# Optimization experiments

Hardware: AMD Instinct MI355X
Metric: run time of the kernel (lower is better)

## Reference

```python
import jax, jax.numpy as jnp
import numpy as np

B, S, D = 8, 1024, 1024
H, HD = 16, 64  # multiheads, head_dim; H*HD == D


def setup_inputs() -> dict:
    key = jax.random.key(0)
    ks = jax.random.split(key, 6)
    mk = lambda k, shape, scale=1.0: (jax.random.normal(k, shape, dtype=jnp.float32) * scale)
    return {
        "Q_seq": mk(ks[0], (B, S, D)),
        "K_seq": mk(ks[1], (B, S, D)),
        "V_seq": mk(ks[2], (B, S, D)),
        # nn.Linear weights stored as (out_features, in_features)
        "WQ": mk(ks[3], (H * HD, D), scale=D ** -0.5),
        "WK": mk(ks[4], (H * HD, D), scale=D ** -0.5),
        "WV": mk(ks[5], (H * HD, D), scale=D ** -0.5),
    }


def _attn(Q_seq, K_seq, V_seq, WQ, WK, WV):
    # projections (Linear: x @ W.T), then split heads -> [B, H, S, HD]
    def proj(x, W):
        y = jnp.einsum('bsd,od->bso', x, W)
        return y.reshape(x.shape[0], -1, H, HD).transpose(0, 2, 1, 3)
    Q, K, V = proj(Q_seq, WQ), proj(K_seq, WK), proj(V_seq, WV)
    scale = 1.0 / jnp.sqrt(jnp.float32(HD))
    scores = jnp.einsum('bhqd,bhkd->bhqk', Q, K) * scale  # [B,H,S,S]
    attn = jax.nn.softmax(scores, axis=-1)
    # dropout p=0.1 is identity in eval mode
    out = jnp.einsum('bhqk,bhkd->bhqd', attn, V)
    return out.transpose(0, 2, 1, 3).reshape(out.shape[0], -1, H * HD)


def reference(Q_seq, K_seq, V_seq, WQ, WK, WV):
    return _attn(Q_seq, K_seq, V_seq, WQ, WK, WV)
```

## Files before the change

kernel.cpp:

```cpp
#include <hip/hip_runtime.h>
#include <stdint.h>


#define B_N 8
#define S_N 1024
#define D_N 1024
#define H_N 16
#define HD_N 64
#define M_N (B_N * S_N)

typedef __bf16 bfrag __attribute__((ext_vector_type(8)));
typedef float f32x4 __attribute__((ext_vector_type(4)));
typedef float f32x16 __attribute__((ext_vector_type(16)));
typedef unsigned int u32;
typedef u32 u32x2 __attribute__((ext_vector_type(2)));
typedef unsigned short u16;

__device__ __forceinline__ u16 f2bf(float f) {
  uint32_t u = __float_as_uint(f);
  u += 0x7FFFu + ((u >> 16) & 1u);
  return (u16)(u >> 16);
}

__device__ __forceinline__ void gl_lds16(const void* g, void* l) {
  __builtin_amdgcn_global_load_lds(
      (const __attribute__((address_space(1))) uint32_t*)g,
      (__attribute__((address_space(3))) uint32_t*)l, 16, 0, 0);
}

__device__ __forceinline__ u32 cvtpk(float lo, float hi) {
  u32 r;
  asm("v_cvt_pk_bf16_f32 %0, %1, %2" : "=v"(r) : "v"(lo), "v"(hi));
  return r;
}

__device__ __forceinline__ u32x2 pl32swap(u32 a, u32 b) {
#if __has_builtin(__builtin_amdgcn_permlane32_swap)
  return __builtin_amdgcn_permlane32_swap(a, b, false, false);
#else
  u32 sa = (u32)__shfl_xor((int)a, 32, 64), sb = (u32)__shfl_xor((int)b, 32, 64);
  const bool hi = (threadIdx.x & 32) != 0;
  u32x2 r;
  r[0] = hi ? sb : a;
  r[1] = hi ? b : sa;
  return r;
#endif
}

__device__ __forceinline__ float xhalf_max(float v) {
  u32x2 r = pl32swap(__float_as_uint(v), __float_as_uint(v));
  return fmaxf(__uint_as_float(r[0]), __uint_as_float(r[1]));
}
__device__ __forceinline__ float xhalf_add(float v) {
  u32x2 r = pl32swap(__float_as_uint(v), __float_as_uint(v));
  return __uint_as_float(r[0]) + __uint_as_float(r[1]);
}

__global__ void cvt3(const float* __restrict__ s0, const float* __restrict__ s1,
                     const float* __restrict__ s2, u16* __restrict__ d0,
                     u16* __restrict__ d1, u16* __restrict__ d2, int n4) {
  const float* s = blockIdx.y == 0 ? s0 : (blockIdx.y == 1 ? s1 : s2);
  u16* d = blockIdx.y == 0 ? d0 : (blockIdx.y == 1 ? d1 : d2);
  int i = blockIdx.x * 256 + threadIdx.x;
  if (i < n4) {
    float4 v = ((const float4*)s)[i];
    ushort4 o;
    o.x = f2bf(v.x); o.y = f2bf(v.y); o.z = f2bf(v.z); o.w = f2bf(v.w);
    ((ushort4*)d)[i] = o;
  }
}

__global__ __launch_bounds__(512, 1) void gemm_qkv(const u16* __restrict__ Xbf,
                                                   const u16* __restrict__ Wbf,
                                                   u16* __restrict__ Ybf) {
  const int bid = blockIdx.x;
  const int wid = (bid & 7) * 96 + (bid >> 3);
  const int mat = wid >> 8;
  const int rem = wid & 255;
  const int m0 = (rem >> 3) * 256;
  const int n0 = (rem & 7) * 128;

  const u16* A = Xbf + (size_t)mat * (M_N * D_N);
  const u16* Bw = Wbf + (size_t)mat * (D_N * D_N);
  u16* Y = Ybf + (size_t)mat * (M_N * D_N);

  __shared__ u16 Ast[3][4][4096];
  __shared__ u16 Bst[3][2][4096];

  const int t = threadIdx.x;
  const int w = t >> 6, l = t & 63;
  const int lr = l & 15, lg = l >> 4;
  const int wm = w >> 1, wn = w & 1;

  const int swcol = (((t & 7) ^ ((t >> 3) & 7)) << 3);
  const u16* aSrc = A + (size_t)(m0 + (t >> 3)) * D_N + swcol;
  const u16* bSrc = Bw + (size_t)(n0 + (t >> 3)) * D_N + swcol;

  const int asw = (lr & 7) << 3;
  const int koff0 = (lg * 8) ^ asw;
  const int koff1 = (32 + lg * 8) ^ asw;

#define STA(buf, c, tt)                                                       \
  gl_lds16(aSrc + (size_t)((c)*64) * D_N + (tt)*64, &Ast[buf][c][t * 8])
#define STB(buf, c, tt)                                                       \
  gl_lds16(bSrc + (size_t)((c)*64) * D_N + (tt)*64, &Bst[buf][c][t * 8])
#define LDA8(AR, buf)                                                         \
  do {                                                                        \
    const u16* p_ = &Ast[buf][wm][lr * 64];                                   \
    _Pragma("unroll") for (int mf_ = 0; mf_ < 4; ++mf_) {                     \
      AR[mf_][0] = *(const bfrag*)(p_ + mf_ * 1024 + koff0);                  \
      AR[mf_][1] = *(const bfrag*)(p_ + mf_ * 1024 + koff1);                  \
    }                                                                         \
  } while (0)
#define LDB4(BR, buf, h)                                                      \
  do {                                                                        \
    const u16* p_ = &Bst[buf][wn][((h)*32 + lr) * 64];                        \
    BR[0][0] = *(const bfrag*)(p_ + koff0);                                   \
    BR[0][1] = *(const bfrag*)(p_ + koff1);                                   \
    BR[1][0] = *(const bfrag*)(p_ + 1024 + koff0);                            \
    BR[1][1] = *(const bfrag*)(p_ + 1024 + koff1);                            \
  } while (0)
#define MMAH(h, AR, BR)                                                       \
  do {                                                                        \
    __builtin_amdgcn_s_setprio(1);                                            \
    _Pragma("unroll") for (int mf_ = 0; mf_ < 4; ++mf_)                       \
    _Pragma("unroll") for (int j_ = 0; j_ < 2; ++j_)                          \
    _Pragma("unroll") for (int kk_ = 0; kk_ < 2; ++kk_)                       \
      acc[mf_][(h)*2 + j_] = __builtin_amdgcn_mfma_f32_16x16x32_bf16(         \
          AR[mf_][kk_], BR[j_][kk_], acc[mf_][(h)*2 + j_], 0, 0, 0);          \
    __builtin_amdgcn_s_setprio(0);                                            \
  } while (0)
#define BARR()                                                                \
  __builtin_amdgcn_s_barrier();                                               \
  __builtin_amdgcn_sched_barrier(0)
#define WAITL()                                                               \
  asm volatile("s_waitcnt lgkmcnt(0)" ::: "memory");                          \
  __builtin_amdgcn_sched_barrier(0)
#define WAITV(n)                                                              \
  asm volatile("s_waitcnt vmcnt(" #n ")" ::: "memory");                       \
  __builtin_amdgcn_sched_barrier(0)

  f32x4 acc[4][4];
#pragma unroll
  for (int i = 0; i < 4; ++i)
#pragma unroll
    for (int j = 0; j < 4; ++j) acc[i][j] = (f32x4){0.f, 0.f, 0.f, 0.f};

  STA(0, 0, 0); STA(0, 1, 0); STA(0, 2, 0); STA(0, 3, 0);
  STB(0, 0, 0); STB(0, 1, 0);
  STA(1, 0, 1); STA(1, 1, 1); STA(1, 2, 1); STA(1, 3, 1);
  STB(1, 0, 1); STB(1, 1, 1);
  WAITV(6);
  BARR();

  int rd = 0, sg = 2;
  for (int kt = 0; kt < 16; ++kt) {
    const bool st = (kt < 14);
    bfrag a[4][2], b[2][2];
    LDA8(a, rd);
    LDB4(b, rd, 0);
    if (st) { STA(sg, 0, kt + 2); STA(sg, 1, kt + 2); STA(sg, 2, kt + 2); }
    BARR(); WAITL();
    MMAH(0, a, b);
    BARR();
    LDB4(b, rd, 1);
    if (st) { STA(sg, 3, kt + 2); STB(sg, 0, kt + 2); STB(sg, 1, kt + 2); }
    BARR(); WAITL();
    MMAH(1, a, b);
    if (kt < 14) { WAITV(6); } else if (kt == 14) { WAITV(0); }
    BARR();
    rd = (rd == 2) ? 0 : rd + 1;
    sg = (sg == 2) ? 0 : sg + 1;
  }

  const float alpha = (mat == 0) ? 0.18033688011112042f : 1.0f;
  const int mrow = m0 + wm * 64;
  const int ncol = n0 + wn * 64;
  if (mat < 2) {
#pragma unroll
    for (int mf = 0; mf < 4; ++mf) {
      const int row0 = mrow + mf * 16 + lg * 4;
#pragma unroll
      for (int nf = 0; nf < 4; ++nf) {
        const int col = ncol + nf * 16 + lr;
#pragma unroll
        for (int r = 0; r < 4; ++r)
          Y[(size_t)(row0 + r) * D_N + col] = f2bf(acc[mf][nf][r] * alpha);
      }
    }
  } else {
    const int b = m0 >> 10;
#pragma unroll
    for (int mf = 0; mf < 4; ++mf) {
      const int s0 = (m0 & 1023) + wm * 64 + mf * 16 + lg * 4;
#pragma unroll
      for (int nf = 0; nf < 4; ++nf) {
        const int col = ncol + nf * 16 + lr;
        const f32x4 v = acc[mf][nf];
        ushort4 pk;
        pk.x = f2bf(v[0]); pk.y = f2bf(v[1]);
        pk.z = f2bf(v[2]); pk.w = f2bf(v[3]);
        *(ushort4*)(Y + (size_t)(b * D_N + col) * S_N + s0) = pk;
      }
    }
  }
#undef STA
#undef STB
#undef LDA8
#undef LDB4
#undef MMAH
#undef BARR
#undef WAITL
#undef WAITV
}

union AttnSMem {
  struct { u16 K[3][4096]; u16 V[3][4096]; } st;
  float ol[4][32 * 34];
};

__global__ __launch_bounds__(256, 3) void attn_fwd(const u16* __restrict__ Yq,
                                                   const u16* __restrict__ Yk,
                                                   const u16* __restrict__ Yv,
                                                   float* __restrict__ out) {
  const int bid = blockIdx.x;
  const int wid = (bid & 7) * 128 + (bid >> 3);
  const int qt = wid & 7, bh = wid >> 3;
  const int b = bh >> 4, h = bh & 15;
  const int t = threadIdx.x, w = t >> 6, l = t & 63;
  const int ln = l & 31, hi = l >> 5;

  __shared__ AttnSMem sm;

  const int qbase = qt * 128 + w * 32;

  const int row0 = w * 8 + (l >> 3);
  const int srcoff = (((l & 7) ^ ((l >> 3) & 7)) << 3);
  const u16* kS0 = Yk + ((size_t)(b * S_N + row0) * D_N + h * HD_N + srcoff);
  const u16* vS0 = Yv + ((size_t)(b * D_N + h * HD_N + row0) * S_N + srcoff);

#define STAGE(buf, tt)                                                        \
  do {                                                                        \
    const u16* ka_ = kS0 + (size_t)(tt) * 64 * D_N;                           \
    const u16* va_ = vS0 + (tt) * 64;                                         \
    gl_lds16(ka_, sm.st.K[buf] + w * 512);                                    \
    gl_lds16(ka_ + (size_t)32 * D_N, sm.st.K[buf] + 2048 + w * 512);          \
    gl_lds16(va_, sm.st.V[buf] + w * 512);                                    \
    gl_lds16(va_ + (size_t)32 * S_N, sm.st.V[buf] + 2048 + w * 512);          \
  } while (0)

  bfrag qf[4];
  {
    const u16* qp = Yq + ((size_t)(b * S_N + qbase + ln) * D_N + h * HD_N + hi * 8);
#pragma unroll
    for (int c = 0; c < 4; ++c) qf[c] = *(const bfrag*)(qp + c * 16);
  }

  STAGE(0, 0);
  STAGE(1, 1);

  int kcol[4];
#pragma unroll
  for (int c = 0; c < 4; ++c)
    kcol[c] = (((c * 32 + hi * 16) ^ ((ln & 7) << 4)) >> 1);

  f32x16 o0, o1;
#pragma unroll
  for (int r = 0; r < 16; ++r) { o0[r] = 0.f; o1[r] = 0.f; }
  float m_r = -3.0e38f, l_r = 0.f;

  asm volatile("s_waitcnt vmcnt(4)" ::: "memory");
  __builtin_amdgcn_sched_barrier(0);
  __builtin_amdgcn_s_barrier();

  int rd = 0, sb = 2;
  for (int kt = 0; kt < 16; ++kt) {
    if (kt < 14) STAGE(sb, kt + 2);

    const u16* Kb = sm.st.K[rd];
    const u16* Vb = sm.st.V[rd];

    bfrag kf[8];
#pragma unroll
    for (int s2 = 0; s2 < 2; ++s2)
#pragma unroll
      for (int c = 0; c < 4; ++c)
        kf[s2 * 4 + c] = *(const bfrag*)(Kb + (s2 * 32 + ln) * 64 + kcol[c]);

    f32x16 sa, sbv;
#pragma unroll
    for (int r = 0; r < 16; ++r) { sa[r] = 0.f; sbv[r] = 0.f; }
    __builtin_amdgcn_s_setprio(1);
#pragma unroll
    for (int c = 0; c < 4; ++c) {
      sa = __builtin_amdgcn_mfma_f32_32x32x16_bf16(kf[c], qf[c], sa, 0, 0, 0);
      sbv = __builtin_amdgcn_mfma_f32_32x32x16_bf16(kf[4 + c], qf[c], sbv, 0, 0, 0);
    }
    __builtin_amdgcn_s_setprio(0);

    bfrag vf[8];
#pragma unroll
    for (int hf = 0; hf < 2; ++hf)
#pragma unroll
      for (int c = 0; c < 4; ++c)
        vf[hf * 4 + c] = *(const bfrag*)(Vb + (hf * 32 + ln) * 64 + kcol[c]);

    float t16[16];
#pragma unroll
    for (int r = 0; r < 16; ++r) t16[r] = fmaxf(sa[r], sbv[r]);
    float t8[8];
#pragma unroll
    for (int r = 0; r < 8; ++r) t8[r] = fmaxf(t16[r], t16[r + 8]);
    float t4[4];
#pragma unroll
    for (int r = 0; r < 4; ++r) t4[r] = fmaxf(t8[r], t8[r + 4]);
    float pmax = fmaxf(fmaxf(t4[0], t4[1]), fmaxf(t4[2], t4[3]));
    pmax = xhalf_max(pmax);

    if (__any(pmax > m_r + 8.f)) {
      const float mnew = fmaxf(m_r, pmax);
      const float corr = exp2f(m_r - mnew);
#pragma unroll
      for (int r = 0; r < 16; ++r) { o0[r] *= corr; o1[r] *= corr; }
      l_r *= corr;
      m_r = mnew;
    }

#pragma unroll
    for (int r = 0; r < 16; ++r) sa[r] = exp2f(sa[r] - m_r);
#pragma unroll
    for (int r = 0; r < 16; ++r) sbv[r] = exp2f(sbv[r] - m_r);
    float s16[16];
#pragma unroll
    for (int r = 0; r < 16; ++r) s16[r] = sa[r] + sbv[r];
    float s8[8];
#pragma unroll
    for (int r = 0; r < 8; ++r) s8[r] = s16[r] + s16[r + 8];
    float s4[4];
#pragma unroll
    for (int r = 0; r < 4; ++r) s4[r] = s8[r] + s8[r + 4];
    float rsum = (s4[0] + s4[1]) + (s4[2] + s4[3]);
    l_r += xhalf_add(rsum);

    __builtin_amdgcn_s_setprio(1);
#pragma unroll
    for (int c = 0; c < 4; ++c) {
      const int bs = (c & 1) * 8;
      float p0, p1, p2, p3, p4, p5, p6, p7;
      if (c < 2) {
        p0 = sa[bs + 0]; p1 = sa[bs + 1]; p2 = sa[bs + 2]; p3 = sa[bs + 3];
        p4 = sa[bs + 4]; p5 = sa[bs + 5]; p6 = sa[bs + 6]; p7 = sa[bs + 7];
      } else {
        p0 = sbv[bs + 0]; p1 = sbv[bs + 1]; p2 = sbv[bs + 2]; p3 = sbv[bs + 3];
        p4 = sbv[bs + 4]; p5 = sbv[bs + 5]; p6 = sbv[bs + 6]; p7 = sbv[bs + 7];
      }
      const u32 x1 = cvtpk(p0, p1), x2 = cvtpk(p2, p3);
      const u32 y1 = cvtpk(p4, p5), y2 = cvtpk(p6, p7);
      const u32x2 s1 = pl32swap(x1, y1);
      const u32x2 s2 = pl32swap(x2, y2);
      union { u32 u[4]; bfrag v; } pu;
      pu.u[0] = s1[0]; pu.u[1] = s2[0]; pu.u[2] = s1[1]; pu.u[3] = s2[1];
      o0 = __builtin_amdgcn_mfma_f32_32x32x16_bf16(vf[c], pu.v, o0, 0, 0, 0);
      o1 = __builtin_amdgcn_mfma_f32_32x32x16_bf16(vf[4 + c], pu.v, o1, 0, 0, 0);
    }
    __builtin_amdgcn_s_setprio(0);

    if (kt < 14) {
      asm volatile("s_waitcnt vmcnt(4)" ::: "memory");
    } else {
      asm volatile("s_waitcnt vmcnt(0)" ::: "memory");
    }
    __builtin_amdgcn_sched_barrier(0);
    __builtin_amdgcn_s_barrier();

    rd = (rd == 2) ? 0 : rd + 1;
    sb = (sb == 2) ? 0 : sb + 1;
  }

  const float inv = 1.f / l_r;
  float* ow = sm.ol[w];
  const int qr = l >> 1, ch = l & 1;
  const float* rp = ow + qr * 34 + ch * 16;
  float* op = out + ((size_t)(b * S_N + qbase + qr) * D_N + h * HD_N + ch * 16);

#pragma unroll
  for (int g = 0; g < 4; ++g) {
    f32x4 v;
#pragma unroll
    for (int j = 0; j < 4; ++j) v[j] = o0[g * 4 + j] * inv;
    *(f32x4*)(ow + ln * 34 + g * 8 + hi * 4) = v;
  }
  asm volatile("s_waitcnt lgkmcnt(0)" ::: "memory");
  __builtin_amdgcn_sched_barrier(0);
#pragma unroll
  for (int j = 0; j < 4; ++j)
    *(f32x4*)(op + j * 4) = *(const f32x4*)(rp + j * 4);
  asm volatile("s_waitcnt lgkmcnt(0)" ::: "memory");
  __builtin_amdgcn_sched_barrier(0);

#pragma unroll
  for (int g = 0; g < 4; ++g) {
    f32x4 v;
#pragma unroll
    for (int j = 0; j < 4; ++j) v[j] = o1[g * 4 + j] * inv;
    *(f32x4*)(ow + ln * 34 + g * 8 + hi * 4) = v;
  }
  asm volatile("s_waitcnt lgkmcnt(0)" ::: "memory");
  __builtin_amdgcn_sched_barrier(0);
#pragma unroll
  for (int j = 0; j < 4; ++j)
    *(f32x4*)(op + 32 + j * 4) = *(const f32x4*)(rp + j * 4);
#undef STAGE
}

extern "C" void kernel_launch(void* const* d_in, const int* in_sizes, int n_in,
                              void* d_out, int out_size, void* d_ws, size_t ws_size,
                              hipStream_t stream) {
  const float* Qs = (const float*)d_in[0];
  const float* Ks = (const float*)d_in[1];
  const float* Vs = (const float*)d_in[2];
  const float* WQ = (const float*)d_in[3];
  const float* WK = (const float*)d_in[4];
  const float* WV = (const float*)d_in[5];
  if (ws_size < 106954752ull) return;

  u16* Xbf = (u16*)d_ws;
  u16* Wbf = Xbf + 25165824;
  u16* Ybf = Wbf + 3145728;
  float* out = (float*)d_out;

  cvt3<<<dim3(8192, 3), 256, 0, stream>>>(Qs, Ks, Vs, Xbf, Xbf + 8388608,
                                          Xbf + 16777216, 2097152);
  cvt3<<<dim3(1024, 3), 256, 0, stream>>>(WQ, WK, WV, Wbf, Wbf + 1048576,
                                          Wbf + 2097152, 262144);
  gemm_qkv<<<dim3(768), 512, 0, stream>>>(Xbf, Wbf, Ybf);
  attn_fwd<<<dim3(1024), 256, 0, stream>>>(Ybf, Ybf + 8388608, Ybf + 16777216, out);
}
```

Measured before the change: 159.9 us.

## Fuse fp32-to-bf16 conversion into QKV GEMM loads and use raw exp2

Removes the separate cvt3 kernels. The GEMM now loads fp32 activations and weights into registers, converts them to bf16 with packed cvt instructions, and writes them into swizzled LDS, replacing the async global_load_lds triple-buffer with a register-staged double buffer. This avoids writing and re-reading the bf16 copies in global memory and saves kernel launches. The cost is double the global read bytes inside the GEMM and more register pressure, and the direct-to-LDS async path is lost. The attention kernel also swaps exp2f for the hardware v_exp_f32 intrinsic.

After: 142.7 us. 1.12x faster.

```diff
diff --git a/kernel.cpp b/kernel.cpp
--- a/kernel.cpp
+++ b/kernel.cpp
@@ -14,6 +14,7 @@
 typedef float f32x16 __attribute__((ext_vector_type(16)));
 typedef unsigned int u32;
 typedef u32 u32x2 __attribute__((ext_vector_type(2)));
+typedef u32 u32x4 __attribute__((ext_vector_type(4)));
 typedef unsigned short u16;
 
 __device__ __forceinline__ u16 f2bf(float f) {
@@ -32,6 +33,16 @@
   u32 r;
   asm("v_cvt_pk_bf16_f32 %0, %1, %2" : "=v"(r) : "v"(lo), "v"(hi));
   return r;
+}
+
+__device__ __forceinline__ float exp2r(float x) {
+#if __has_builtin(__builtin_amdgcn_exp2f)
+  return __builtin_amdgcn_exp2f(x);
+#else
+  float r;
+  asm("v_exp_f32 %0, %1" : "=v"(r) : "v"(x));
+  return r;
+#endif
 }
 
 __device__ __forceinline__ u32x2 pl32swap(u32 a, u32 b) {
@@ -56,23 +67,11 @@
   return __uint_as_float(r[0]) + __uint_as_float(r[1]);
 }
 
-__global__ void cvt3(const float* __restrict__ s0, const float* __restrict__ s1,
-                     const float* __restrict__ s2, u16* __restrict__ d0,
-                     u16* __restrict__ d1, u16* __restrict__ d2, int n4) {
-  const float* s = blockIdx.y == 0 ? s0 : (blockIdx.y == 1 ? s1 : s2);
-  u16* d = blockIdx.y == 0 ? d0 : (blockIdx.y == 1 ? d1 : d2);
-  int i = blockIdx.x * 256 + threadIdx.x;
-  if (i < n4) {
-    float4 v = ((const float4*)s)[i];
-    ushort4 o;
-    o.x = f2bf(v.x); o.y = f2bf(v.y); o.z = f2bf(v.z); o.w = f2bf(v.w);
-    ((ushort4*)d)[i] = o;
-  }
-}
-
-__global__ __launch_bounds__(512, 1) void gemm_qkv(const u16* __restrict__ Xbf,
-                                                   const u16* __restrict__ Wbf,
-                                                   u16* __restrict__ Ybf) {
+__global__ __launch_bounds__(512, 1) void gemm_qkv(
+    const float* __restrict__ Qs, const float* __restrict__ Ks,
+    const float* __restrict__ Vs, const float* __restrict__ WQ,
+    const float* __restrict__ WK, const float* __restrict__ WV,
+    u16* __restrict__ Ybf) {
   const int bid = blockIdx.x;
   const int wid = (bid & 7) * 96 + (bid >> 3);
   const int mat = wid >> 8;
@@ -80,30 +79,60 @@
   const int m0 = (rem >> 3) * 256;
   const int n0 = (rem & 7) * 128;
 
-  const u16* A = Xbf + (size_t)mat * (M_N * D_N);
-  const u16* Bw = Wbf + (size_t)mat * (D_N * D_N);
+  const float* A = mat == 0 ? Qs : (mat == 1 ? Ks : Vs);
+  const float* Bw = mat == 0 ? WQ : (mat == 1 ? WK : WV);
   u16* Y = Ybf + (size_t)mat * (M_N * D_N);
 
-  __shared__ u16 Ast[3][4][4096];
-  __shared__ u16 Bst[3][2][4096];
+  __shared__ u16 Ast[2][4][4096];
+  __shared__ u16 Bst[2][2][4096];
 
   const int t = threadIdx.x;
   const int w = t >> 6, l = t & 63;
   const int lr = l & 15, lg = l >> 4;
   const int wm = w >> 1, wn = w & 1;
 
-  const int swcol = (((t & 7) ^ ((t >> 3) & 7)) << 3);
-  const u16* aSrc = A + (size_t)(m0 + (t >> 3)) * D_N + swcol;
-  const u16* bSrc = Bw + (size_t)(n0 + (t >> 3)) * D_N + swcol;
+  const float* aSrc = A + (size_t)(m0 + (t >> 3)) * D_N + (t & 7) * 8;
+  const float* bSrc = Bw + (size_t)(n0 + (t >> 3)) * D_N + (t & 7) * 8;
+  const int dst8 = (t >> 3) * 64 + ((((t & 7) ^ ((t >> 3) & 7))) << 3);
 
   const int asw = (lr & 7) << 3;
   const int koff0 = (lg * 8) ^ asw;
   const int koff1 = (32 + lg * 8) ^ asw;
 
-#define STA(buf, c, tt)                                                       \
-  gl_lds16(aSrc + (size_t)((c)*64) * D_N + (tt)*64, &Ast[buf][c][t * 8])
-#define STB(buf, c, tt)                                                       \
-  gl_lds16(bSrc + (size_t)((c)*64) * D_N + (tt)*64, &Bst[buf][c][t * 8])
+  float4 ra[4][2], rw[2][2];
+
+#define LOADT(tt)                                                             \
+  do {                                                                        \
+    _Pragma("unroll") for (int c_ = 0; c_ < 4; ++c_) {                        \
+      ra[c_][0] = *(const float4*)(aSrc + (size_t)(c_ * 64) * D_N + (tt)*64); \
+      ra[c_][1] =                                                             \
+          *(const float4*)(aSrc + (size_t)(c_ * 64) * D_N + (tt)*64 + 4);     \
+    }                                                                         \
+    _Pragma("unroll") for (int c_ = 0; c_ < 2; ++c_) {                        \
+      rw[c_][0] = *(const float4*)(bSrc + (size_t)(c_ * 64) * D_N + (tt)*64); \
+      rw[c_][1] =                                                             \
+          *(const float4*)(bSrc + (size_t)(c_ * 64) * D_N + (tt)*64 + 4);     \
+    }                                                                         \
+  } while (0)
+#define WRITET(buf)                                                           \
+  do {                                                                        \
+    _Pragma("unroll") for (int c_ = 0; c_ < 4; ++c_) {                        \
+      u32x4 pk_;                                                              \
+      pk_[0] = cvtpk(ra[c_][0].x, ra[c_][0].y);                               \
+      pk_[1] = cvtpk(ra[c_][0].z, ra[c_][0].w);                               \
+      pk_[2] = cvtpk(ra[c_][1].x, ra[c_][1].y);                               \
+      pk_[3] = cvtpk(ra[c_][1].z, ra[c_][1].w);                               \
+      *(u32x4*)(&Ast[buf][c_][dst8]) = pk_;                                   \
+    }                                                                         \
+    _Pragma("unroll") for (int c_ = 0; c_ < 2; ++c_) {                        \
+      u32x4 pk_;                                                              \
+      pk_[0] = cvtpk(rw[c_][0].x, rw[c_][0].y);                               \
+      pk_[1] = cvtpk(rw[c_][0].z, rw[c_][0].w);                               \
+      pk_[2] = cvtpk(rw[c_][1].x, rw[c_][1].y);                               \
+      pk_[3] = cvtpk(rw[c_][1].z, rw[c_][1].w);                               \
+      *(u32x4*)(&Bst[buf][c_][dst8]) = pk_;                                   \
+    }                                                                         \
+  } while (0)
 #define LDA8(AR, buf)                                                         \
   do {                                                                        \
     const u16* p_ = &Ast[buf][wm][lr * 64];                                   \
@@ -136,8 +165,8 @@
 #define WAITL()                                                               \
   asm volatile("s_waitcnt lgkmcnt(0)" ::: "memory");                          \
   __builtin_amdgcn_sched_barrier(0)
-#define WAITV(n)                                                              \
-  asm volatile("s_waitcnt vmcnt(" #n ")" ::: "memory");                       \
+#define WAITV0()                                                              \
+  asm volatile("s_waitcnt vmcnt(0)" ::: "memory");                            \
   __builtin_amdgcn_sched_barrier(0)
 
   f32x4 acc[4][4];
@@ -146,31 +175,29 @@
 #pragma unroll
     for (int j = 0; j < 4; ++j) acc[i][j] = (f32x4){0.f, 0.f, 0.f, 0.f};
 
-  STA(0, 0, 0); STA(0, 1, 0); STA(0, 2, 0); STA(0, 3, 0);
-  STB(0, 0, 0); STB(0, 1, 0);
-  STA(1, 0, 1); STA(1, 1, 1); STA(1, 2, 1); STA(1, 3, 1);
-  STB(1, 0, 1); STB(1, 1, 1);
-  WAITV(6);
+  LOADT(0);
+  WAITV0();
+  WRITET(0);
+  LOADT(1);
+  WAITL();
   BARR();
 
-  int rd = 0, sg = 2;
   for (int kt = 0; kt < 16; ++kt) {
-    const bool st = (kt < 14);
+    const int cb = kt & 1;
     bfrag a[4][2], b[2][2];
-    LDA8(a, rd);
-    LDB4(b, rd, 0);
-    if (st) { STA(sg, 0, kt + 2); STA(sg, 1, kt + 2); STA(sg, 2, kt + 2); }
-    BARR(); WAITL();
+    LDA8(a, cb);
+    LDB4(b, cb, 0);
+    if (kt < 15) {
+      WAITV0();
+      WRITET(cb ^ 1);
+      if (kt < 14) LOADT(kt + 2);
+    }
+    WAITL();
     MMAH(0, a, b);
+    LDB4(b, cb, 1);
+    WAITL();
+    MMAH(1, a, b);
     BARR();
-    LDB4(b, rd, 1);
-    if (st) { STA(sg, 3, kt + 2); STB(sg, 0, kt + 2); STB(sg, 1, kt + 2); }
-    BARR(); WAITL();
-    MMAH(1, a, b);
-    if (kt < 14) { WAITV(6); } else if (kt == 14) { WAITV(0); }
-    BARR();
-    rd = (rd == 2) ? 0 : rd + 1;
-    sg = (sg == 2) ? 0 : sg + 1;
   }
 
   const float alpha = (mat == 0) ? 0.18033688011112042f : 1.0f;
@@ -204,14 +231,14 @@
       }
     }
   }
-#undef STA
-#undef STB
+#undef LOADT
+#undef WRITET
 #undef LDA8
 #undef LDB4
 #undef MMAH
 #undef BARR
 #undef WAITL
-#undef WAITV
+#undef WAITV0
 }
 
 union AttnSMem {
@@ -319,7 +346,7 @@
 
     if (__any(pmax > m_r + 8.f)) {
       const float mnew = fmaxf(m_r, pmax);
-      const float corr = exp2f(m_r - mnew);
+      const float corr = exp2r(m_r - mnew);
 #pragma unroll
       for (int r = 0; r < 16; ++r) { o0[r] *= corr; o1[r] *= corr; }
       l_r *= corr;
@@ -327,9 +354,9 @@
     }
 
 #pragma unroll
-    for (int r = 0; r < 16; ++r) sa[r] = exp2f(sa[r] - m_r);
-#pragma unroll
-    for (int r = 0; r < 16; ++r) sbv[r] = exp2f(sbv[r] - m_r);
+    for (int r = 0; r < 16; ++r) sa[r] = exp2r(sa[r] - m_r);
+#pragma unroll
+    for (int r = 0; r < 16; ++r) sbv[r] = exp2r(sbv[r] - m_r);
     float s16[16];
 #pragma unroll
     for (int r = 0; r < 16; ++r) s16[r] = sa[r] + sbv[r];
@@ -422,17 +449,11 @@
   const float* WQ = (const float*)d_in[3];
   const float* WK = (const float*)d_in[4];
   const float* WV = (const float*)d_in[5];
-  if (ws_size < 106954752ull) return;
-
-  u16* Xbf = (u16*)d_ws;
-  u16* Wbf = Xbf + 25165824;
-  u16* Ybf = Wbf + 3145728;
+  if (ws_size < 50331648ull) return;
+
+  u16* Ybf = (u16*)d_ws;
   float* out = (float*)d_out;
 
-  cvt3<<<dim3(8192, 3), 256, 0, stream>>>(Qs, Ks, Vs, Xbf, Xbf + 8388608,
-                                          Xbf + 16777216, 2097152);
-  cvt3<<<dim3(1024, 3), 256, 0, stream>>>(WQ, WK, WV, Wbf, Wbf + 1048576,
-                                          Wbf + 2097152, 262144);
-  gemm_qkv<<<dim3(768), 512, 0, stream>>>(Xbf, Wbf, Ybf);
+  gemm_qkv<<<dim3(768), 512, 0, stream>>>(Qs, Ks, Vs, WQ, WK, WV, Ybf);
   attn_fwd<<<dim3(1024), 256, 0, stream>>>(Ybf, Ybf + 8388608, Ybf + 16777216, out);
 }
```
